# Kernel tuning notes

Hardware: AMD Instinct MI355X
Metric: run time of the kernel (lower is better)

The kernel has to match this reference:

```python
import jax, jax.numpy as jnp
import numpy as np

NUM_HEADS = 16


def setup_inputs() -> dict:
    key = jax.random.key(0)
    k1, k2, k3 = jax.random.split(key, 3)
    T, B, E = 2048, 2, 1024
    x = jax.random.normal(k1, (T, B, E), dtype=jnp.float32)
    in_proj_w = jax.random.normal(k2, (E, 3 * E), dtype=jnp.float32) * (E ** -0.5)
    in_proj_b = jnp.zeros((3 * E,), dtype=jnp.float32)
    out_w = jax.random.normal(k3, (E, E), dtype=jnp.float32) * (E ** -0.5)
    out_b = jnp.zeros((E,), dtype=jnp.float32)
    return {"x": x, "in_proj_w": in_proj_w, "in_proj_b": in_proj_b,
            "out_w": out_w, "out_b": out_b}


def reference(x, in_proj_w, in_proj_b, out_w, out_b):
    # x: (tgt_len, bsz, embed_dim) -- seq-first, self-attention (q is k is v)
    T, B, E = x.shape
    H = NUM_HEADS
    D = E // H
    scaling = D ** -0.5
    # packed in-projection: einsum('bne,ef->bnf') over (T,B,E)
    proj = jnp.einsum('tbe,ef->tbf', x, in_proj_w) + in_proj_b
    q, k, v = jnp.split(proj, 3, axis=-1)  # each (T, B, E)
    # reshape to (T, B*H, D) then transpose to (B*H, T, D)
    q = q.reshape(T, B * H, D).transpose(1, 0, 2)
    k = k.reshape(T, B * H, D).transpose(1, 0, 2)
    v = v.reshape(T, B * H, D).transpose(1, 0, 2)
    # full O(T^2) attention matrix, scaling applied after QK^T as in source
    attn = jnp.einsum('bie,bje->bij', q, k) * scaling  # (B*H, T, T)
    attn = jax.nn.softmax(attn, axis=-1)
    out = jnp.einsum('bij,bje->bie', attn, v)  # (B*H, T, D)
    # faithful to source: reshape directly (no head transpose-back)
    out = out.reshape(B, T, E)
    out = jnp.einsum('bte,ef->btf', out, out_w) + out_b
    return out
```

## Files before the change

kernel.cpp:

```cpp
#include <hip/hip_runtime.h>
#include <stdint.h>

#define TSEQ 2048
#define NB 2
#define EMB 1024
#define NHEAD 16
#define HDIM 64
#define NT (TSEQ / 64)
#define QSCALE 0.18033688f

typedef __bf16 bf16x8 __attribute__((ext_vector_type(8)));
typedef __bf16 bf16x4 __attribute__((ext_vector_type(4)));
typedef float f32x4 __attribute__((ext_vector_type(4)));
typedef float f32x16 __attribute__((ext_vector_type(16)));
typedef unsigned int u32x4 __attribute__((ext_vector_type(4)));

__device__ __forceinline__ void gload_lds16(const void* g, void* lds) {
    __builtin_amdgcn_global_load_lds(
        (const __attribute__((address_space(1))) unsigned int*)g,
        (__attribute__((address_space(3))) unsigned int*)lds, 16, 0, 0);
}

__device__ __forceinline__ float fast_exp2(float x) {
#if __has_builtin(__builtin_amdgcn_exp2f)
    return __builtin_amdgcn_exp2f(x);
#else
    return exp2f(x);
#endif
}

__device__ __forceinline__ unsigned cvt_pk_bf16(float lo, float hi) {
    unsigned r;
    asm("v_cvt_pk_bf16_f32 %0, %1, %2" : "=v"(r) : "v"(lo), "v"(hi));
    return r;
}

__device__ __forceinline__ void swap32(unsigned& a, unsigned& b) {
    asm("v_permlane32_swap_b32 %0, %1" : "+v"(a), "+v"(b));
}

__device__ __forceinline__ bf16x8 as_bf16x8(u32x4 u) {
    union { u32x4 u; bf16x8 h; } c;
    c.u = u;
    return c.h;
}

__global__ __launch_bounds__(256) void prep_kernel(
    const float* __restrict__ x, const float* __restrict__ w_in,
    const float* __restrict__ w_out,
    __bf16* __restrict__ xb, __bf16* __restrict__ wiT, __bf16* __restrict__ whT)
{
    __shared__ float tile[32][33];
    int bid = blockIdx.x;
    const int tid = threadIdx.x;
    if (bid < 4096) {
        const size_t idx = ((size_t)bid * 256 + tid) * 4;
        float4 v = *(const float4*)(x + idx);
        bf16x4 o = { (__bf16)v.x, (__bf16)v.y, (__bf16)v.z, (__bf16)v.w };
        *(bf16x4*)(xb + idx) = o;
        return;
    }
    bid -= 4096;
    int bx = bid & 127;
    const int by = bid >> 7;
    const float* src; __bf16* dst; int sn;
    if (bx < 96) { src = w_in;  dst = wiT; sn = 3072; }
    else         { bx -= 96; src = w_out; dst = whT; sn = 1024; }
    const int tx = tid & 31, ty = tid >> 5;
    #pragma unroll
    for (int i = 0; i < 4; ++i)
        tile[ty + i * 8][tx] = src[(size_t)(by * 32 + ty + i * 8) * sn + bx * 32 + tx];
    __syncthreads();
    #pragma unroll
    for (int i = 0; i < 4; ++i) {
        float v = tile[tx][ty + i * 8];
        dst[(size_t)(bx * 32 + ty + i * 8) * 1024 + by * 32 + tx] = (__bf16)v;
    }
}

__global__ __launch_bounds__(256) void gemm_qkv_kernel(
    const __bf16* __restrict__ A, const __bf16* __restrict__ BT,
    const float* __restrict__ bias,
    __bf16* __restrict__ Oq, __bf16* __restrict__ Ok, __bf16* __restrict__ Ov)
{
    __shared__ __align__(16) __bf16 As[128 * 64];
    __shared__ __align__(16) __bf16 Bs[128 * 64];
    const int tid = threadIdx.x;
    const int wave = tid >> 6, lane = tid & 63;
    const int l16 = lane & 15, quad = lane >> 4;
    const int wm = wave >> 1, wn = wave & 1;
    const int m0 = blockIdx.y * 128, n0 = blockIdx.x * 128;

    f32x4 acc[4][4];
    #pragma unroll
    for (int mt = 0; mt < 4; ++mt)
        #pragma unroll
        for (int nt = 0; nt < 4; ++nt)
            #pragma unroll
            for (int r = 0; r < 4; ++r) acc[mt][nt][r] = 0.f;

    int smrow[4], schunk[4], sbase[4];
    #pragma unroll
    for (int i = 0; i < 4; ++i) {
        int linear = (wave * 4 + i) * 64 + lane;
        smrow[i] = linear >> 3;
        schunk[i] = (linear & 7) ^ (smrow[i] & 7);
        sbase[i] = (wave * 4 + i) * 512;
    }

    for (int k0 = 0; k0 < 1024; k0 += 64) {
        #pragma unroll
        for (int i = 0; i < 4; ++i) {
            gload_lds16(A + (size_t)(m0 + smrow[i]) * 1024 + k0 + schunk[i] * 8,
                        As + sbase[i]);
            gload_lds16(BT + (size_t)(n0 + smrow[i]) * 1024 + k0 + schunk[i] * 8,
                        Bs + sbase[i]);
        }
        __syncthreads();
        #pragma unroll
        for (int kk = 0; kk < 2; ++kk) {
            bf16x8 am[4], bn[4];
            #pragma unroll
            for (int mt = 0; mt < 4; ++mt) {
                int row = wm * 64 + mt * 16 + l16;
                int c = (kk * 4 + quad) ^ (row & 7);
                am[mt] = *(const bf16x8*)(As + row * 64 + c * 8);
            }
            #pragma unroll
            for (int nt = 0; nt < 4; ++nt) {
                int row = wn * 64 + nt * 16 + l16;
                int c = (kk * 4 + quad) ^ (row & 7);
                bn[nt] = *(const bf16x8*)(Bs + row * 64 + c * 8);
            }
            #pragma unroll
            for (int mt = 0; mt < 4; ++mt)
                #pragma unroll
                for (int nt = 0; nt < 4; ++nt)
                    acc[mt][nt] = __builtin_amdgcn_mfma_f32_16x16x32_bf16(
                        am[mt], bn[nt], acc[mt][nt], 0, 0, 0);
        }
        __syncthreads();
    }

    #pragma unroll
    for (int nt = 0; nt < 4; ++nt) {
        const int col = n0 + wn * 64 + nt * 16 + l16;
        const float bv = bias[col];
        const int sec = col >> 10, f = col & 1023;
        const int h = f >> 6, d = f & 63;
        #pragma unroll
        for (int mt = 0; mt < 4; ++mt)
            #pragma unroll
            for (int r = 0; r < 4; ++r) {
                const int row = m0 + wm * 64 + mt * 16 + quad * 4 + r;
                float v = acc[mt][nt][r] + bv;
                const int t = row >> 1, b = row & 1;
                const int bh = b * NHEAD + h;
                const size_t idx = ((size_t)bh * TSEQ + t) * HDIM + d;
                if (sec == 0)
                    Oq[idx] = (__bf16)(v * QSCALE);
                else if (sec == 1)
                    Ok[idx] = (__bf16)v;
                else
                    Ov[idx] = (__bf16)v;
            }
    }
}

__global__ __launch_bounds__(256) void vtrans_kernel(
    const __bf16* __restrict__ V, __bf16* __restrict__ Vt)
{
    __shared__ __bf16 T[64 * 67];
    const int bh = blockIdx.y;
    const int t0 = blockIdx.x * 64;
    const int tid = threadIdx.x;
    const int r = tid >> 2;
    const int c = (tid & 3) * 16;
    const __bf16* src = V + ((size_t)bh * TSEQ + t0 + r) * HDIM + c;
    bf16x8 a = *(const bf16x8*)src;
    bf16x8 b = *(const bf16x8*)(src + 8);
    #pragma unroll
    for (int j = 0; j < 8; ++j) {
        T[r * 67 + c + j] = a[j];
        T[r * 67 + c + 8 + j] = b[j];
    }
    __syncthreads();
    const int dr = tid >> 2;
    const int tc = (tid & 3) * 16;
    bf16x8 o0, o1;
    #pragma unroll
    for (int j = 0; j < 8; ++j) {
        o0[j] = T[(tc + j) * 67 + dr];
        o1[j] = T[(tc + 8 + j) * 67 + dr];
    }
    __bf16* dst = Vt + ((size_t)bh * HDIM + dr) * TSEQ + t0 + tc;
    *(bf16x8*)dst = o0;
    *(bf16x8*)(dst + 8) = o1;
}

__global__ __launch_bounds__(256, 2) void attn_mfma_kernel(
    const __bf16* __restrict__ Q, const __bf16* __restrict__ K,
    const __bf16* __restrict__ Vt, __bf16* __restrict__ Ob)
{
    __shared__ __align__(16) __bf16 Ks[2][64 * 64];
    __shared__ __align__(16) __bf16 Vs[2][64 * 64];
    __shared__ float Linv[4][32];

    const int tid  = threadIdx.x;
    const int wave = tid >> 6;
    const int lane = tid & 63;
    const int l31  = lane & 31;
    const int hi   = lane >> 5;
    const int m7   = l31 & 7;

    const int lid = blockIdx.x;
    const int xcd = lid & 7;
    const int j   = lid >> 3;
    const int bh  = xcd * 4 + (j >> 4);
    const int qb  = j & 15;

    const int q0 = qb * 128 + wave * 32;

    bf16x8 qf[4];
    {
        const __bf16* Qrow = Q + ((size_t)bh * TSEQ + q0 + l31) * HDIM + 8 * hi;
        #pragma unroll
        for (int c = 0; c < 4; ++c)
            qf[c] = *(const bf16x8*)(Qrow + 16 * c);
    }

    f32x16 Oacc[2];
    #pragma unroll
    for (int dt = 0; dt < 2; ++dt)
        #pragma unroll
        for (int r = 0; r < 16; ++r) Oacc[dt][r] = 0.f;
    float l4[4] = {0.f, 0.f, 0.f, 0.f};

    const __bf16* Kbase = K + (size_t)bh * TSEQ * HDIM;
    const __bf16* Vbase = Vt + (size_t)bh * HDIM * TSEQ;

    int srow[2], schk[2];
    #pragma unroll
    for (int i = 0; i < 2; ++i) {
        const int s = wave * 2 + i;
        srow[i] = s * 8 + (lane >> 3);
        schk[i] = (lane & 7) ^ (srow[i] & 7);
    }

#define STAGE(buf, kt)                                                        \
    {                                                                         \
        _Pragma("unroll")                                                     \
        for (int i = 0; i < 2; ++i) {                                         \
            const int s = wave * 2 + i;                                       \
            gload_lds16(Kbase + (size_t)((kt) * 64 + srow[i]) * HDIM          \
                            + schk[i] * 8,                                    \
                        &Ks[buf][s * 512]);                                   \
            gload_lds16(Vbase + (size_t)srow[i] * TSEQ + (kt) * 64            \
                            + schk[i] * 8,                                    \
                        &Vs[buf][s * 512]);                                   \
        }                                                                     \
    }

    STAGE(0, 0);

    for (int kt = 0; kt < NT; ++kt) {
        const int b = kt & 1;
        __syncthreads();
        if (kt + 1 < NT) STAGE(b ^ 1, kt + 1);

        u32x4 pa[4];
        #pragma unroll
        for (int s = 0; s < 2; ++s) {
            f32x16 sacc;
            #pragma unroll
            for (int r = 0; r < 16; ++r) sacc[r] = 0.f;
            #pragma unroll
            for (int c = 0; c < 4; ++c) {
                bf16x8 kf = *(const bf16x8*)(
                    &Ks[b][(32 * s + l31) * 64 + (((c << 1) | hi) ^ m7) * 8]);
                sacc = __builtin_amdgcn_mfma_f32_32x32x16_bf16(
                    kf, qf[c], sacc, 0, 0, 0);
            }
            float p[16];
            #pragma unroll
            for (int r = 0; r < 16; ++r) {
                p[r] = fast_exp2(sacc[r]);
                l4[r & 3] += p[r];
            }
            unsigned x[8];
            #pragma unroll
            for (int i = 0; i < 8; ++i)
                x[i] = cvt_pk_bf16(p[2 * i], p[2 * i + 1]);
            swap32(x[0], x[2]); swap32(x[1], x[3]);
            swap32(x[4], x[6]); swap32(x[5], x[7]);
            pa[2 * s][0] = x[0]; pa[2 * s][1] = x[1];
            pa[2 * s][2] = x[2]; pa[2 * s][3] = x[3];
            pa[2 * s + 1][0] = x[4]; pa[2 * s + 1][1] = x[5];
            pa[2 * s + 1][2] = x[6]; pa[2 * s + 1][3] = x[7];
        }

        #pragma unroll
        for (int dt = 0; dt < 2; ++dt)
            #pragma unroll
            for (int ks = 0; ks < 4; ++ks) {
                bf16x8 vf = *(const bf16x8*)(
                    &Vs[b][(dt * 32 + l31) * 64 + (((ks << 1) | hi) ^ m7) * 8]);
                Oacc[dt] = __builtin_amdgcn_mfma_f32_32x32x16_bf16(
                    as_bf16x8(pa[ks]), vf, Oacc[dt], 0, 0, 0);
            }
    }
#undef STAGE

    {
        float v = (l4[0] + l4[1]) + (l4[2] + l4[3]);
        v += __shfl_xor(v, 32);
        if (hi == 0)
            Linv[wave][l31] = 1.f / v;
    }
    __syncthreads();

    const size_t base = ((size_t)bh * TSEQ + q0) * HDIM;
    #pragma unroll
    for (int dt = 0; dt < 2; ++dt)
        #pragma unroll
        for (int r = 0; r < 16; ++r) {
            const int ql = (r & 3) + 8 * (r >> 2) + 4 * hi;
            const float inv = Linv[wave][ql];
            Ob[base + (size_t)ql * HDIM + dt * 32 + l31] =
                (__bf16)(Oacc[dt][r] * inv);
        }
}

__global__ __launch_bounds__(256) void gemm_out_kernel(
    const __bf16* __restrict__ A, const __bf16* __restrict__ BT,
    const float* __restrict__ bias, float* __restrict__ out)
{
    __shared__ __align__(16) __bf16 As[64 * 64];
    __shared__ __align__(16) __bf16 Bs[64 * 64];
    const int tid = threadIdx.x;
    const int wave = tid >> 6, lane = tid & 63;
    const int l16 = lane & 15, quad = lane >> 4;
    const int wm = wave >> 1, wn = wave & 1;
    const int m0 = blockIdx.y * 64, n0 = blockIdx.x * 64;

    f32x4 acc[2][2];
    #pragma unroll
    for (int mt = 0; mt < 2; ++mt)
        #pragma unroll
        for (int nt = 0; nt < 2; ++nt)
            #pragma unroll
            for (int r = 0; r < 4; ++r) acc[mt][nt][r] = 0.f;

    int srow[2], schk[2], sbase[2];
    #pragma unroll
    for (int i = 0; i < 2; ++i) {
        const int s = wave * 2 + i;
        srow[i] = s * 8 + (lane >> 3);
        schk[i] = (lane & 7) ^ (srow[i] & 7);
        sbase[i] = s * 512;
    }

    for (int k0 = 0; k0 < 1024; k0 += 64) {
        #pragma unroll
        for (int i = 0; i < 2; ++i) {
            gload_lds16(A + (size_t)(m0 + srow[i]) * 1024 + k0 + schk[i] * 8,
                        As + sbase[i]);
            gload_lds16(BT + (size_t)(n0 + srow[i]) * 1024 + k0 + schk[i] * 8,
                        Bs + sbase[i]);
        }
        __syncthreads();
        #pragma unroll
        for (int kk = 0; kk < 2; ++kk) {
            bf16x8 am[2], bn[2];
            #pragma unroll
            for (int mt = 0; mt < 2; ++mt) {
                int row = wm * 32 + mt * 16 + l16;
                int c = (kk * 4 + quad) ^ (row & 7);
                am[mt] = *(const bf16x8*)(As + row * 64 + c * 8);
            }
            #pragma unroll
            for (int nt = 0; nt < 2; ++nt) {
                int row = wn * 32 + nt * 16 + l16;
                int c = (kk * 4 + quad) ^ (row & 7);
                bn[nt] = *(const bf16x8*)(Bs + row * 64 + c * 8);
            }
            #pragma unroll
            for (int mt = 0; mt < 2; ++mt)
                #pragma unroll
                for (int nt = 0; nt < 2; ++nt)
                    acc[mt][nt] = __builtin_amdgcn_mfma_f32_16x16x32_bf16(
                        am[mt], bn[nt], acc[mt][nt], 0, 0, 0);
        }
        __syncthreads();
    }

    #pragma unroll
    for (int nt = 0; nt < 2; ++nt) {
        const int col = n0 + wn * 32 + nt * 16 + l16;
        const float bv = bias[col];
        #pragma unroll
        for (int mt = 0; mt < 2; ++mt)
            #pragma unroll
            for (int r = 0; r < 4; ++r) {
                const int row = m0 + wm * 32 + mt * 16 + quad * 4 + r;
                out[(size_t)row * 1024 + col] = acc[mt][nt][r] + bv;
            }
    }
}

extern "C" void kernel_launch(void* const* d_in, const int* in_sizes, int n_in,
                              void* d_out, int out_size, void* d_ws, size_t ws_size,
                              hipStream_t stream) {
    const float* x     = (const float*)d_in[0];
    const float* w_in  = (const float*)d_in[1];
    const float* b_in  = (const float*)d_in[2];
    const float* w_out = (const float*)d_in[3];
    const float* b_out = (const float*)d_in[4];
    float* out = (float*)d_out;

    const size_t M1 = (size_t)1024 * 1024;
    __bf16* ws  = (__bf16*)d_ws;
    __bf16* xb  = ws;
    __bf16* wiT = xb  + 4 * M1;
    __bf16* whT = wiT + 3 * M1;
    __bf16* Qb  = whT + 1 * M1;
    __bf16* Kb  = Qb  + 4 * M1;
    __bf16* Vt  = Kb  + 4 * M1;
    __bf16* Vb  = (__bf16*)d_out;
    __bf16* Ob  = xb;

    prep_kernel<<<8192, 256, 0, stream>>>(x, w_in, w_out, xb, wiT, whT);
    gemm_qkv_kernel<<<dim3(24, 32), 256, 0, stream>>>(
        xb, wiT, b_in, Qb, Kb, Vb);
    vtrans_kernel<<<dim3(32, 32), 256, 0, stream>>>(Vb, Vt);
    attn_mfma_kernel<<<dim3(512), 256, 0, stream>>>(
        Qb, Kb, Vt, Ob);
    gemm_out_kernel<<<dim3(16, 64), 256, 0, stream>>>(
        Ob, whT, b_out, out);
}
```

Baseline: 190.9 us.

## Fuse V transpose into QKV GEMM epilogue and enlarge out-GEMM M tile

The QKV GEMM epilogue now writes V directly in transposed (d-major) layout by staging the tile through shared memory, which removes the separate vtrans kernel launch and its extra global read and write of V. Q/K sections branch once per block instead of per element. The output projection GEMM tile grows from 64x64 to 128x64, halving its grid and increasing reuse of the weight tile, at the cost of more registers and less parallelism.

```diff
diff --git a/kernel.cpp b/kernel.cpp
--- a/kernel.cpp
+++ b/kernel.cpp
@@ -81,10 +81,13 @@
 __global__ __launch_bounds__(256) void gemm_qkv_kernel(
     const __bf16* __restrict__ A, const __bf16* __restrict__ BT,
     const float* __restrict__ bias,
-    __bf16* __restrict__ Oq, __bf16* __restrict__ Ok, __bf16* __restrict__ Ov)
+    __bf16* __restrict__ Oq, __bf16* __restrict__ Ok, __bf16* __restrict__ Vt)
 {
-    __shared__ __align__(16) __bf16 As[128 * 64];
-    __shared__ __align__(16) __bf16 Bs[128 * 64];
+    __shared__ __align__(16) char smem[128 * 131 * 2];
+    __bf16* As = (__bf16*)smem;
+    __bf16* Bs = (__bf16*)(smem + 16384);
+    __bf16* Tt = (__bf16*)smem;
+
     const int tid = threadIdx.x;
     const int wave = tid >> 6, lane = tid & 63;
     const int l16 = lane & 15, quad = lane >> 4;
@@ -142,60 +145,57 @@
         __syncthreads();
     }
 
-    #pragma unroll
-    for (int nt = 0; nt < 4; ++nt) {
-        const int col = n0 + wn * 64 + nt * 16 + l16;
-        const float bv = bias[col];
-        const int sec = col >> 10, f = col & 1023;
-        const int h = f >> 6, d = f & 63;
-        #pragma unroll
-        for (int mt = 0; mt < 4; ++mt)
-            #pragma unroll
-            for (int r = 0; r < 4; ++r) {
-                const int row = m0 + wm * 64 + mt * 16 + quad * 4 + r;
-                float v = acc[mt][nt][r] + bv;
-                const int t = row >> 1, b = row & 1;
-                const int bh = b * NHEAD + h;
-                const size_t idx = ((size_t)bh * TSEQ + t) * HDIM + d;
-                if (sec == 0)
-                    Oq[idx] = (__bf16)(v * QSCALE);
-                else if (sec == 1)
-                    Ok[idx] = (__bf16)v;
-                else
-                    Ov[idx] = (__bf16)v;
-            }
-    }
-}
-
-__global__ __launch_bounds__(256) void vtrans_kernel(
-    const __bf16* __restrict__ V, __bf16* __restrict__ Vt)
-{
-    __shared__ __bf16 T[64 * 67];
-    const int bh = blockIdx.y;
-    const int t0 = blockIdx.x * 64;
-    const int tid = threadIdx.x;
-    const int r = tid >> 2;
-    const int c = (tid & 3) * 16;
-    const __bf16* src = V + ((size_t)bh * TSEQ + t0 + r) * HDIM + c;
-    bf16x8 a = *(const bf16x8*)src;
-    bf16x8 b = *(const bf16x8*)(src + 8);
-    #pragma unroll
-    for (int j = 0; j < 8; ++j) {
-        T[r * 67 + c + j] = a[j];
-        T[r * 67 + c + 8 + j] = b[j];
-    }
-    __syncthreads();
-    const int dr = tid >> 2;
-    const int tc = (tid & 3) * 16;
-    bf16x8 o0, o1;
-    #pragma unroll
-    for (int j = 0; j < 8; ++j) {
-        o0[j] = T[(tc + j) * 67 + dr];
-        o1[j] = T[(tc + 8 + j) * 67 + dr];
-    }
-    __bf16* dst = Vt + ((size_t)bh * HDIM + dr) * TSEQ + t0 + tc;
-    *(bf16x8*)dst = o0;
-    *(bf16x8*)(dst + 8) = o1;
+    const int sec = n0 >> 10;
+    if (sec < 2) {
+        __bf16* __restrict__ O = (sec == 0) ? Oq : Ok;
+        const float scale = (sec == 0) ? QSCALE : 1.f;
+        #pragma unroll
+        for (int nt = 0; nt < 4; ++nt) {
+            const int col = n0 + wn * 64 + nt * 16 + l16;
+            const float bv = bias[col];
+            const int f = col & 1023;
+            const int h = f >> 6, d = f & 63;
+            #pragma unroll
+            for (int mt = 0; mt < 4; ++mt)
+                #pragma unroll
+                for (int r = 0; r < 4; ++r) {
+                    const int row = m0 + wm * 64 + mt * 16 + quad * 4 + r;
+                    const float v = (acc[mt][nt][r] + bv) * scale;
+                    const int t = row >> 1, b = row & 1;
+                    const int bh = b * NHEAD + h;
+                    O[((size_t)bh * TSEQ + t) * HDIM + d] = (__bf16)v;
+                }
+        }
+    } else {
+        #pragma unroll
+        for (int nt = 0; nt < 4; ++nt) {
+            const int lc = wn * 64 + nt * 16 + l16;
+            const float bv = bias[n0 + lc];
+            #pragma unroll
+            for (int mt = 0; mt < 4; ++mt)
+                #pragma unroll
+                for (int r = 0; r < 4; ++r) {
+                    const int ml = wm * 64 + mt * 16 + quad * 4 + r;
+                    Tt[ml * 131 + lc] = (__bf16)(acc[mt][nt][r] + bv);
+                }
+        }
+        __syncthreads();
+        const int b = wave & 1, hl = wave >> 1;
+        const int bh = b * NHEAD + ((n0 - 2048) >> 6) + hl;
+        const int t0g = m0 >> 1;
+        __bf16* dstbase = Vt + (size_t)bh * HDIM * TSEQ + t0g;
+        const int dq = lane >> 3;
+        const int tb = (lane & 7) * 8;
+        #pragma unroll
+        for (int p = 0; p < 8; ++p) {
+            const int d = dq + 8 * p;
+            bf16x8 o;
+            #pragma unroll
+            for (int jj = 0; jj < 8; ++jj)
+                o[jj] = Tt[(2 * (tb + jj) + b) * 131 + hl * 64 + d];
+            *(bf16x8*)(dstbase + (size_t)d * TSEQ + tb) = o;
+        }
+    }
 }
 
 __global__ __launch_bounds__(256, 2) void attn_mfma_kernel(
@@ -335,46 +335,55 @@
     const __bf16* __restrict__ A, const __bf16* __restrict__ BT,
     const float* __restrict__ bias, float* __restrict__ out)
 {
-    __shared__ __align__(16) __bf16 As[64 * 64];
+    __shared__ __align__(16) __bf16 As[128 * 64];
     __shared__ __align__(16) __bf16 Bs[64 * 64];
     const int tid = threadIdx.x;
     const int wave = tid >> 6, lane = tid & 63;
     const int l16 = lane & 15, quad = lane >> 4;
     const int wm = wave >> 1, wn = wave & 1;
-    const int m0 = blockIdx.y * 64, n0 = blockIdx.x * 64;
-
-    f32x4 acc[2][2];
-    #pragma unroll
-    for (int mt = 0; mt < 2; ++mt)
+    const int m0 = blockIdx.y * 128, n0 = blockIdx.x * 64;
+
+    f32x4 acc[4][2];
+    #pragma unroll
+    for (int mt = 0; mt < 4; ++mt)
         #pragma unroll
         for (int nt = 0; nt < 2; ++nt)
             #pragma unroll
             for (int r = 0; r < 4; ++r) acc[mt][nt][r] = 0.f;
 
-    int srow[2], schk[2], sbase[2];
+    int amrow[4], amchk[4], ambase[4];
+    #pragma unroll
+    for (int i = 0; i < 4; ++i) {
+        int linear = (wave * 4 + i) * 64 + lane;
+        amrow[i] = linear >> 3;
+        amchk[i] = (linear & 7) ^ (amrow[i] & 7);
+        ambase[i] = (wave * 4 + i) * 512;
+    }
+    int brow[2], bchk[2], bbase[2];
     #pragma unroll
     for (int i = 0; i < 2; ++i) {
         const int s = wave * 2 + i;
-        srow[i] = s * 8 + (lane >> 3);
-        schk[i] = (lane & 7) ^ (srow[i] & 7);
-        sbase[i] = s * 512;
+        brow[i] = s * 8 + (lane >> 3);
+        bchk[i] = (lane & 7) ^ (brow[i] & 7);
+        bbase[i] = s * 512;
     }
 
     for (int k0 = 0; k0 < 1024; k0 += 64) {
         #pragma unroll
-        for (int i = 0; i < 2; ++i) {
-            gload_lds16(A + (size_t)(m0 + srow[i]) * 1024 + k0 + schk[i] * 8,
-                        As + sbase[i]);
-            gload_lds16(BT + (size_t)(n0 + srow[i]) * 1024 + k0 + schk[i] * 8,
-                        Bs + sbase[i]);
-        }
+        for (int i = 0; i < 4; ++i)
+            gload_lds16(A + (size_t)(m0 + amrow[i]) * 1024 + k0 + amchk[i] * 8,
+                        As + ambase[i]);
+        #pragma unroll
+        for (int i = 0; i < 2; ++i)
+            gload_lds16(BT + (size_t)(n0 + brow[i]) * 1024 + k0 + bchk[i] * 8,
+                        Bs + bbase[i]);
         __syncthreads();
         #pragma unroll
         for (int kk = 0; kk < 2; ++kk) {
-            bf16x8 am[2], bn[2];
-            #pragma unroll
-            for (int mt = 0; mt < 2; ++mt) {
-                int row = wm * 32 + mt * 16 + l16;
+            bf16x8 am[4], bn[2];
+            #pragma unroll
+            for (int mt = 0; mt < 4; ++mt) {
+                int row = wm * 64 + mt * 16 + l16;
                 int c = (kk * 4 + quad) ^ (row & 7);
                 am[mt] = *(const bf16x8*)(As + row * 64 + c * 8);
             }
@@ -385,7 +394,7 @@
                 bn[nt] = *(const bf16x8*)(Bs + row * 64 + c * 8);
             }
             #pragma unroll
-            for (int mt = 0; mt < 2; ++mt)
+            for (int mt = 0; mt < 4; ++mt)
                 #pragma unroll
                 for (int nt = 0; nt < 2; ++nt)
                     acc[mt][nt] = __builtin_amdgcn_mfma_f32_16x16x32_bf16(
@@ -399,10 +408,10 @@
         const int col = n0 + wn * 32 + nt * 16 + l16;
         const float bv = bias[col];
         #pragma unroll
-        for (int mt = 0; mt < 2; ++mt)
+        for (int mt = 0; mt < 4; ++mt)
             #pragma unroll
             for (int r = 0; r < 4; ++r) {
-                const int row = m0 + wm * 32 + mt * 16 + quad * 4 + r;
+                const int row = m0 + wm * 64 + mt * 16 + quad * 4 + r;
                 out[(size_t)row * 1024 + col] = acc[mt][nt][r] + bv;
             }
     }
@@ -426,15 +435,13 @@
     __bf16* Qb  = whT + 1 * M1;
     __bf16* Kb  = Qb  + 4 * M1;
     __bf16* Vt  = Kb  + 4 * M1;
-    __bf16* Vb  = (__bf16*)d_out;
     __bf16* Ob  = xb;
 
     prep_kernel<<<8192, 256, 0, stream>>>(x, w_in, w_out, xb, wiT, whT);
     gemm_qkv_kernel<<<dim3(24, 32), 256, 0, stream>>>(
-        xb, wiT, b_in, Qb, Kb, Vb);
-    vtrans_kernel<<<dim3(32, 32), 256, 0, stream>>>(Vb, Vt);
+        xb, wiT, b_in, Qb, Kb, Vt);
     attn_mfma_kernel<<<dim3(512), 256, 0, stream>>>(
         Qb, Kb, Vt, Ob);
-    gemm_out_kernel<<<dim3(16, 64), 256, 0, stream>>>(
+    gemm_out_kernel<<<dim3(16, 32), 256, 0, stream>>>(
         Ob, whT, b_out, out);
 }
```

Measured after the change: 184.3 us. 3.5% less time.
